# Optimization experiments

Measured on AMD Instinct MI355X. Metric: run time of the kernel, lower is better.

Reference implementation:

```python
import jax, jax.numpy as jnp
import numpy as np

NA, NT, A_DIM, E_DIM, L_LABELS, STEPS = 1024, 1024, 128, 128, 128, 2


def setup_inputs() -> dict:
    key = jax.random.key(0)
    k1, k2, k3, k4, k5 = jax.random.split(key, 5)
    return {
        "inputs": jax.random.randint(k1, (NA, NT), 0, L_LABELS, dtype=jnp.int32),
        "first_a": jax.random.normal(k2, (NA, A_DIM), dtype=jnp.float32),
        "first_t": jax.random.normal(k3, (NT, E_DIM), dtype=jnp.float32),
        "Awij": jax.random.normal(k4, (L_LABELS, A_DIM, E_DIM), dtype=jnp.float32),
        "Awij2": jax.random.normal(k5, (L_LABELS, E_DIM, A_DIM), dtype=jnp.float32),
    }


def _mp_step(update_a, update_t, inputs, Awij, Awij2):
    L = Awij.shape[0]
    # Phase A: a[j] += sum_t update_t[t] @ Awij2[inputs[j, t]]
    # Pre-contract task states with every label's weight matrix, then use
    # per-label 0/1 adjacency masks as dense GEMMs (compute-bound form of the
    # per-edge gather-multiply-accumulate in the original while loops).
    t_proj = jnp.einsum('te,lea->tla', update_t, Awij2)  # [Nt, L, A]

    def body_a(acc, l):
        mask = (inputs == l).astype(update_a.dtype)      # [Na, Nt]
        return acc + mask @ t_proj[:, l, :], None

    msg_a, _ = jax.lax.scan(body_a, jnp.zeros_like(update_a), jnp.arange(L))
    new_a = update_a + msg_a

    # Phase T: t[k] += sum_j new_a[j] @ Awij[inputs[j, k]] (uses updated a,
    # matching the loop order in the original body)
    a_proj = jnp.einsum('ja,lae->jle', new_a, Awij)      # [Na, L, E]

    def body_t(acc, l):
        mask = (inputs == l).astype(update_t.dtype)      # [Na, Nt]
        return acc + mask.T @ a_proj[:, l, :], None

    msg_t, _ = jax.lax.scan(body_t, jnp.zeros_like(update_t), jnp.arange(L))
    return new_a, update_t + msg_t


def reference(inputs, first_a, first_t, Awij, Awij2):
    a, t = first_a, first_t
    for _ in range(STEPS):
        a, t = _mp_step(a, t, inputs, Awij, Awij2)
    na, a_dim = a.shape
    nt, e_dim = t.shape
    top = jnp.concatenate([a, jnp.zeros((na, e_dim), a.dtype)], axis=1)
    bot = jnp.concatenate([t, jnp.zeros((nt, a_dim), t.dtype)], axis=1)
    return jnp.concatenate([top, bot], axis=0)  # [Na+Nt, A+E]
```

## Files before the change

kernel.cpp:

```cpp
#include <hip/hip_runtime.h>
#include <hip/hip_bf16.h>
#include <stdint.h>


typedef short bf16x8 __attribute__((ext_vector_type(8)));
typedef float f32x4  __attribute__((ext_vector_type(4)));

#define GLD16(g, l) __builtin_amdgcn_global_load_lds( \
    (const __attribute__((address_space(1))) void*)(uintptr_t)(g), \
    (__attribute__((address_space(3))) void*)(uintptr_t)(l), 16, 0, 0)

#define BF_LO(v) __uint_as_float((v) << 16)
#define BF_HI(v) __uint_as_float((v) & 0xffff0000u)

static __device__ __forceinline__ uint32_t pk2(float lo, float hi) {
    __hip_bfloat16 h0 = __float2bfloat16(lo), h1 = __float2bfloat16(hi);
    return ((uint32_t)(*(uint16_t*)&h1) << 16) | (uint32_t)(*(uint16_t*)&h0);
}

__global__ __launch_bounds__(256) void transpose_int_kernel(const int* __restrict__ in,
                                                            int* __restrict__ out) {
    __shared__ int tile[32][33];
    int b = blockIdx.x;
    int tr = b >> 5, tc = b & 31;
    int r0 = tr * 32, c0 = tc * 32;
    int tx = threadIdx.x & 31, ty = threadIdx.x >> 5;
#pragma unroll
    for (int p = 0; p < 4; ++p)
        tile[ty + p * 8][tx] = in[(size_t)(r0 + ty + p * 8) * 1024 + c0 + tx];
    __syncthreads();
#pragma unroll
    for (int p = 0; p < 4; ++p) {
        int cc = ty + p * 8;
        out[(size_t)(c0 + cc) * 1024 + r0 + tx] = tile[tx][cc];
    }
}

__global__ __launch_bounds__(256) void transpose_w_kernel(const float* __restrict__ W2,
                                                          const float* __restrict__ W1,
                                                          uint16_t* __restrict__ O2T,
                                                          uint16_t* __restrict__ O1T) {
    __shared__ float tile[32][33];
    int b = blockIdx.x;
    const float* W = W2;
    uint16_t* O = O2T;
    if (b >= 2048) { b -= 2048; W = W1; O = O1T; }
    int l = b >> 4, sub = b & 15;
    int x0 = (sub >> 2) * 32, y0 = (sub & 3) * 32;
    int tx = threadIdx.x & 31, ty = threadIdx.x >> 5;
#pragma unroll
    for (int p = 0; p < 4; ++p)
        tile[ty + p * 8][tx] = W[(size_t)l * 16384 + (size_t)(x0 + ty + p * 8) * 128 + y0 + tx];
    __syncthreads();
#pragma unroll
    for (int p = 0; p < 4; ++p) {
        int yy = ty + p * 8;
        __hip_bfloat16 h = __float2bfloat16(tile[tx][yy]);
        O[(size_t)(l * 128 + y0 + yy) * 128 + x0 + tx] = *(uint16_t*)&h;
    }
}

__global__ __launch_bounds__(256) void init_out_kernel(const float* __restrict__ fa,
                                                       const float* __restrict__ ft,
                                                       float* __restrict__ out,
                                                       uint16_t* __restrict__ srcAb,
                                                       uint16_t* __restrict__ srcTb) {
    int i = blockIdx.x * 256 + threadIdx.x;
    int r = i >> 8, c = i & 255;
    float v = 0.f;
    if (c < 128) {
        v = (r < 1024) ? fa[(size_t)r * 128 + c] : ft[(size_t)(r - 1024) * 128 + c];
        __hip_bfloat16 h = __float2bfloat16(v);
        if (r < 1024) srcAb[(size_t)r * 128 + c] = *(uint16_t*)&h;
        else          srcTb[(size_t)(r - 1024) * 128 + c] = *(uint16_t*)&h;
    }
    out[i] = v;
}

__global__ __launch_bounds__(512, 2) void proj_kernel(const uint16_t* __restrict__ src,
                                                      const uint16_t* __restrict__ WT,
                                                      uint16_t* __restrict__ proj) {
    __shared__ uint16_t At[128 * 128];
    __shared__ uint16_t Bt[128 * 128];

    const int tid = threadIdx.x;
    const int lane = tid & 63, wv = tid >> 6;
    const int bid = blockIdx.x;
    const int virt = (bid & 7) * 128 + (bid >> 3);
    const int mt = virt & 7;
    const int nt = virt >> 3;
    const int wr = wv >> 2, wc = wv & 3;

    const int rr = lane >> 4;
    const int sx16 = lane & 15;
#pragma unroll
    for (int g = 0; g < 4; ++g) {
        int row = wv * 16 + g * 4 + rr;
        int sx = sx16 ^ (row & 15);
        GLD16((const char*)src + ((size_t)(mt * 128 + row) * 128 + sx * 8) * 2,
              (char*)At + (wv * 16 + g * 4) * 256);
        GLD16((const char*)WT + ((size_t)(nt * 128 + row) * 128 + sx * 8) * 2,
              (char*)Bt + (wv * 16 + g * 4) * 256);
    }
    __syncthreads();

    f32x4 acc[4][2] = {};
    const int q = lane >> 4, rl = lane & 15;
#pragma unroll
    for (int kk = 0; kk < 4; ++kk) {
        bf16x8 af[4], bfr[2];
#pragma unroll
        for (int m = 0; m < 4; ++m) {
            int row = wr * 64 + m * 16 + rl;
            int sw = (kk * 4 + q) ^ (row & 15);
            af[m] = *(const bf16x8*)((const char*)At + row * 256 + sw * 16);
        }
#pragma unroll
        for (int n = 0; n < 2; ++n) {
            int row = wc * 32 + n * 16 + rl;
            int sw = (kk * 4 + q) ^ (row & 15);
            bfr[n] = *(const bf16x8*)((const char*)Bt + row * 256 + sw * 16);
        }
#pragma unroll
        for (int m = 0; m < 4; ++m)
#pragma unroll
            for (int n = 0; n < 2; ++n)
                acc[m][n] = __builtin_amdgcn_mfma_f32_16x16x32_bf16(bfr[n], af[m], acc[m][n], 0, 0, 0);
    }

#pragma unroll
    for (int m = 0; m < 4; ++m)
#pragma unroll
        for (int n = 0; n < 2; ++n) {
            int mrow = mt * 128 + wr * 64 + m * 16 + rl;
            int ncol = nt * 128 + wc * 32 + n * 16 + q * 4;
            uint2 pk;
            pk.x = pk2(acc[m][n][0], acc[m][n][1]);
            pk.y = pk2(acc[m][n][2], acc[m][n][3]);
            *(uint2*)(proj + (size_t)mrow * 16384 + ncol) = pk;
        }
}

__global__ __launch_bounds__(256, 8) void gather_partial_kernel(
    const int* __restrict__ labels,
    const uint32_t* __restrict__ proj,
    float* __restrict__ partial)
{
    __shared__ uint16_t lab16[128];
    __shared__ float red[4][128];
    const int bid = blockIdx.x;
    const int j = bid >> 3, ts = bid & 7;
    const int tid = threadIdx.x;
    const int lane = tid & 63, wv = tid >> 6;

    if (tid < 128) lab16[tid] = (uint16_t)labels[(size_t)j * 1024 + ts * 128 + tid];
    __syncthreads();

    float a0 = 0.f, a1 = 0.f, b0 = 0.f, b1 = 0.f;
    const uint32_t lane_u = (uint32_t)lane;
    const int t0 = ts * 128 + wv * 32;
#pragma unroll 1
    for (int i = 0; i < 32; i += 8) {
        ushort4 L0 = *(const ushort4*)&lab16[wv * 32 + i];
        ushort4 L1 = *(const ushort4*)&lab16[wv * 32 + i + 4];
        const uint32_t* base = proj + (size_t)(t0 + i) * 8192 + lane_u;
        uint32_t v0 = base[(uint32_t)L0.x * 64];
        uint32_t v1 = base[8192u + (uint32_t)L0.y * 64];
        uint32_t v2 = base[16384u + (uint32_t)L0.z * 64];
        uint32_t v3 = base[24576u + (uint32_t)L0.w * 64];
        uint32_t v4 = base[32768u + (uint32_t)L1.x * 64];
        uint32_t v5 = base[40960u + (uint32_t)L1.y * 64];
        uint32_t v6 = base[49152u + (uint32_t)L1.z * 64];
        uint32_t v7 = base[57344u + (uint32_t)L1.w * 64];
        a0 += BF_LO(v0) + BF_LO(v1) + BF_LO(v2) + BF_LO(v3);
        a1 += BF_HI(v0) + BF_HI(v1) + BF_HI(v2) + BF_HI(v3);
        b0 += BF_LO(v4) + BF_LO(v5) + BF_LO(v6) + BF_LO(v7);
        b1 += BF_HI(v4) + BF_HI(v5) + BF_HI(v6) + BF_HI(v7);
    }
    float2 pr;
    pr.x = a0 + b0;
    pr.y = a1 + b1;
    *(float2*)&red[wv][lane * 2] = pr;
    __syncthreads();

    if (tid < 128) {
        float s = (red[0][tid] + red[1][tid]) + (red[2][tid] + red[3][tid]);
        partial[((size_t)j * 8 + ts) * 128 + tid] = s;
    }
}

__global__ __launch_bounds__(256) void reduce_state_kernel(const float* __restrict__ partial,
                                                           float* __restrict__ state,
                                                           uint16_t* __restrict__ mirror) {
    int i = blockIdx.x * 256 + threadIdx.x;
    int j = i >> 7, c = i & 127;
    const float* p = partial + (size_t)j * 1024 + c;
    float s = ((p[0] + p[128]) + (p[256] + p[384])) + ((p[512] + p[640]) + (p[768] + p[896]));
    float v = state[(size_t)j * 256 + c] + s;
    state[(size_t)j * 256 + c] = v;
    __hip_bfloat16 h = __float2bfloat16(v);
    mirror[(size_t)j * 128 + c] = *(uint16_t*)&h;
}

extern "C" void kernel_launch(void* const* d_in, const int* in_sizes, int n_in,
                              void* d_out, int out_size, void* d_ws, size_t ws_size,
                              hipStream_t stream) {
    const int*   inputs  = (const int*)d_in[0];
    const float* first_a = (const float*)d_in[1];
    const float* first_t = (const float*)d_in[2];
    const float* Awij    = (const float*)d_in[3];
    const float* Awij2   = (const float*)d_in[4];
    float* out = (float*)d_out;

    char* w = (char*)d_ws;
    int*      inputsT = (int*)(w);
    uint16_t* W2T     = (uint16_t*)(w + (4u << 20));
    uint16_t* W1T     = (uint16_t*)(w + (8u << 20));
    uint16_t* srcAb   = (uint16_t*)(w + (12u << 20));
    uint16_t* srcTb   = (uint16_t*)(w + (12u << 20) + (1u << 19));
    float*    partial = (float*)(w + (13u << 20));
    uint16_t* proj16  = (uint16_t*)(w + (20u << 20));
    if (ws_size < (52u << 20)) return;

    float* stateA = out;
    float* stateT = out + 1024 * 256;

    transpose_int_kernel<<<1024, 256, 0, stream>>>(inputs, inputsT);
    transpose_w_kernel<<<4096, 256, 0, stream>>>(Awij2, Awij, W2T, W1T);
    init_out_kernel<<<2048, 256, 0, stream>>>(first_a, first_t, out, srcAb, srcTb);

    for (int s = 0; s < 2; ++s) {
        proj_kernel<<<1024, 512, 0, stream>>>(srcTb, W2T, proj16);
        gather_partial_kernel<<<8192, 256, 0, stream>>>(inputs, (const uint32_t*)proj16, partial);
        reduce_state_kernel<<<512, 256, 0, stream>>>(partial, stateA, srcAb);
        proj_kernel<<<1024, 512, 0, stream>>>(srcAb, W1T, proj16);
        gather_partial_kernel<<<8192, 256, 0, stream>>>(inputsT, (const uint32_t*)proj16, partial);
        reduce_state_kernel<<<512, 256, 0, stream>>>(partial, stateT, srcTb);
    }
}
```

Before: 170.1 us.

## Merge prep kernels, drop proj block swizzle, widen gather loads to 16

Folds the three setup kernels (label transpose, weight transpose and cast, output init) into one launch that branches on block index, which removes two kernel launches and their gaps. Drops the block-index remapping in the projection GEMM so blocks take M tiles in plain order. The gather kernel now issues 16 independent loads per iteration instead of 8, uses readfirstlane to keep the label offsets scalar, and keeps four accumulator pairs. This gives more memory-level parallelism in the gather at the cost of more registers, and changes the L2 locality pattern of the projection kernel.

```diff
diff --git a/kernel.cpp b/kernel.cpp
--- a/kernel.cpp
+++ b/kernel.cpp
@@ -18,63 +18,62 @@
     return ((uint32_t)(*(uint16_t*)&h1) << 16) | (uint32_t)(*(uint16_t*)&h0);
 }
 
-__global__ __launch_bounds__(256) void transpose_int_kernel(const int* __restrict__ in,
-                                                            int* __restrict__ out) {
-    __shared__ int tile[32][33];
-    int b = blockIdx.x;
-    int tr = b >> 5, tc = b & 31;
-    int r0 = tr * 32, c0 = tc * 32;
-    int tx = threadIdx.x & 31, ty = threadIdx.x >> 5;
-#pragma unroll
-    for (int p = 0; p < 4; ++p)
-        tile[ty + p * 8][tx] = in[(size_t)(r0 + ty + p * 8) * 1024 + c0 + tx];
-    __syncthreads();
-#pragma unroll
-    for (int p = 0; p < 4; ++p) {
-        int cc = ty + p * 8;
-        out[(size_t)(c0 + cc) * 1024 + r0 + tx] = tile[tx][cc];
-    }
-}
-
-__global__ __launch_bounds__(256) void transpose_w_kernel(const float* __restrict__ W2,
-                                                          const float* __restrict__ W1,
-                                                          uint16_t* __restrict__ O2T,
-                                                          uint16_t* __restrict__ O1T) {
+__global__ __launch_bounds__(256) void prep_kernel(const int* __restrict__ in,
+                                                   int* __restrict__ inT,
+                                                   const float* __restrict__ W2,
+                                                   const float* __restrict__ W1,
+                                                   uint16_t* __restrict__ O2T,
+                                                   uint16_t* __restrict__ O1T,
+                                                   const float* __restrict__ fa,
+                                                   const float* __restrict__ ft,
+                                                   float* __restrict__ out,
+                                                   uint16_t* __restrict__ srcAb,
+                                                   uint16_t* __restrict__ srcTb) {
     __shared__ float tile[32][33];
     int b = blockIdx.x;
-    const float* W = W2;
-    uint16_t* O = O2T;
-    if (b >= 2048) { b -= 2048; W = W1; O = O1T; }
-    int l = b >> 4, sub = b & 15;
-    int x0 = (sub >> 2) * 32, y0 = (sub & 3) * 32;
     int tx = threadIdx.x & 31, ty = threadIdx.x >> 5;
-#pragma unroll
-    for (int p = 0; p < 4; ++p)
-        tile[ty + p * 8][tx] = W[(size_t)l * 16384 + (size_t)(x0 + ty + p * 8) * 128 + y0 + tx];
-    __syncthreads();
-#pragma unroll
-    for (int p = 0; p < 4; ++p) {
-        int yy = ty + p * 8;
-        __hip_bfloat16 h = __float2bfloat16(tile[tx][yy]);
-        O[(size_t)(l * 128 + y0 + yy) * 128 + x0 + tx] = *(uint16_t*)&h;
-    }
-}
-
-__global__ __launch_bounds__(256) void init_out_kernel(const float* __restrict__ fa,
-                                                       const float* __restrict__ ft,
-                                                       float* __restrict__ out,
-                                                       uint16_t* __restrict__ srcAb,
-                                                       uint16_t* __restrict__ srcTb) {
-    int i = blockIdx.x * 256 + threadIdx.x;
-    int r = i >> 8, c = i & 255;
-    float v = 0.f;
-    if (c < 128) {
-        v = (r < 1024) ? fa[(size_t)r * 128 + c] : ft[(size_t)(r - 1024) * 128 + c];
-        __hip_bfloat16 h = __float2bfloat16(v);
-        if (r < 1024) srcAb[(size_t)r * 128 + c] = *(uint16_t*)&h;
-        else          srcTb[(size_t)(r - 1024) * 128 + c] = *(uint16_t*)&h;
-    }
-    out[i] = v;
+
+    if (b < 1024) {
+        int tr = b >> 5, tc = b & 31;
+        int r0 = tr * 32, c0 = tc * 32;
+#pragma unroll
+        for (int p = 0; p < 4; ++p)
+            tile[ty + p * 8][tx] = __int_as_float(in[(size_t)(r0 + ty + p * 8) * 1024 + c0 + tx]);
+        __syncthreads();
+#pragma unroll
+        for (int p = 0; p < 4; ++p) {
+            int cc = ty + p * 8;
+            inT[(size_t)(c0 + cc) * 1024 + r0 + tx] = __float_as_int(tile[tx][cc]);
+        }
+    } else if (b < 5120) {
+        int bb = b - 1024;
+        const float* W = W2;
+        uint16_t* O = O2T;
+        if (bb >= 2048) { bb -= 2048; W = W1; O = O1T; }
+        int l = bb >> 4, sub = bb & 15;
+        int x0 = (sub >> 2) * 32, y0 = (sub & 3) * 32;
+#pragma unroll
+        for (int p = 0; p < 4; ++p)
+            tile[ty + p * 8][tx] = W[(size_t)l * 16384 + (size_t)(x0 + ty + p * 8) * 128 + y0 + tx];
+        __syncthreads();
+#pragma unroll
+        for (int p = 0; p < 4; ++p) {
+            int yy = ty + p * 8;
+            __hip_bfloat16 h = __float2bfloat16(tile[tx][yy]);
+            O[(size_t)(l * 128 + y0 + yy) * 128 + x0 + tx] = *(uint16_t*)&h;
+        }
+    } else {
+        int i = (b - 5120) * 256 + threadIdx.x;
+        int r = i >> 8, c = i & 255;
+        float v = 0.f;
+        if (c < 128) {
+            v = (r < 1024) ? fa[(size_t)r * 128 + c] : ft[(size_t)(r - 1024) * 128 + c];
+            __hip_bfloat16 h = __float2bfloat16(v);
+            if (r < 1024) srcAb[(size_t)r * 128 + c] = *(uint16_t*)&h;
+            else          srcTb[(size_t)(r - 1024) * 128 + c] = *(uint16_t*)&h;
+        }
+        out[i] = v;
+    }
 }
 
 __global__ __launch_bounds__(512, 2) void proj_kernel(const uint16_t* __restrict__ src,
@@ -86,9 +85,8 @@
     const int tid = threadIdx.x;
     const int lane = tid & 63, wv = tid >> 6;
     const int bid = blockIdx.x;
-    const int virt = (bid & 7) * 128 + (bid >> 3);
-    const int mt = virt & 7;
-    const int nt = virt >> 3;
+    const int mt = bid & 7;
+    const int nt = bid >> 3;
     const int wr = wv >> 2, wc = wv & 3;
 
     const int rr = lane >> 4;
@@ -156,30 +154,39 @@
     if (tid < 128) lab16[tid] = (uint16_t)labels[(size_t)j * 1024 + ts * 128 + tid];
     __syncthreads();
 
+    const uint32_t lane_u = (uint32_t)lane;
+    const uint32_t* tb = proj + (size_t)(ts * 128 + wv * 32) * 8192 + lane_u;
     float a0 = 0.f, a1 = 0.f, b0 = 0.f, b1 = 0.f;
-    const uint32_t lane_u = (uint32_t)lane;
-    const int t0 = ts * 128 + wv * 32;
+    float c0 = 0.f, c1 = 0.f, d0 = 0.f, d1 = 0.f;
+
 #pragma unroll 1
-    for (int i = 0; i < 32; i += 8) {
-        ushort4 L0 = *(const ushort4*)&lab16[wv * 32 + i];
-        ushort4 L1 = *(const ushort4*)&lab16[wv * 32 + i + 4];
-        const uint32_t* base = proj + (size_t)(t0 + i) * 8192 + lane_u;
-        uint32_t v0 = base[(uint32_t)L0.x * 64];
-        uint32_t v1 = base[8192u + (uint32_t)L0.y * 64];
-        uint32_t v2 = base[16384u + (uint32_t)L0.z * 64];
-        uint32_t v3 = base[24576u + (uint32_t)L0.w * 64];
-        uint32_t v4 = base[32768u + (uint32_t)L1.x * 64];
-        uint32_t v5 = base[40960u + (uint32_t)L1.y * 64];
-        uint32_t v6 = base[49152u + (uint32_t)L1.z * 64];
-        uint32_t v7 = base[57344u + (uint32_t)L1.w * 64];
-        a0 += BF_LO(v0) + BF_LO(v1) + BF_LO(v2) + BF_LO(v3);
-        a1 += BF_HI(v0) + BF_HI(v1) + BF_HI(v2) + BF_HI(v3);
-        b0 += BF_LO(v4) + BF_LO(v5) + BF_LO(v6) + BF_LO(v7);
-        b1 += BF_HI(v4) + BF_HI(v5) + BF_HI(v6) + BF_HI(v7);
+    for (int i = 0; i < 32; i += 16) {
+        int L[16];
+#pragma unroll
+        for (int g = 0; g < 4; ++g) {
+            ushort4 q = *(const ushort4*)&lab16[wv * 32 + i + g * 4];
+            L[g * 4 + 0] = __builtin_amdgcn_readfirstlane((int)q.x);
+            L[g * 4 + 1] = __builtin_amdgcn_readfirstlane((int)q.y);
+            L[g * 4 + 2] = __builtin_amdgcn_readfirstlane((int)q.z);
+            L[g * 4 + 3] = __builtin_amdgcn_readfirstlane((int)q.w);
+        }
+        uint32_t v[16];
+#pragma unroll
+        for (int e = 0; e < 16; ++e)
+            v[e] = tb[(uint32_t)(i + e) * 8192u + (uint32_t)L[e] * 64u];
+
+        a0 += BF_LO(v[0]) + BF_LO(v[1]) + BF_LO(v[2]) + BF_LO(v[3]);
+        a1 += BF_HI(v[0]) + BF_HI(v[1]) + BF_HI(v[2]) + BF_HI(v[3]);
+        b0 += BF_LO(v[4]) + BF_LO(v[5]) + BF_LO(v[6]) + BF_LO(v[7]);
+        b1 += BF_HI(v[4]) + BF_HI(v[5]) + BF_HI(v[6]) + BF_HI(v[7]);
+        c0 += BF_LO(v[8]) + BF_LO(v[9]) + BF_LO(v[10]) + BF_LO(v[11]);
+        c1 += BF_HI(v[8]) + BF_HI(v[9]) + BF_HI(v[10]) + BF_HI(v[11]);
+        d0 += BF_LO(v[12]) + BF_LO(v[13]) + BF_LO(v[14]) + BF_LO(v[15]);
+        d1 += BF_HI(v[12]) + BF_HI(v[13]) + BF_HI(v[14]) + BF_HI(v[15]);
     }
     float2 pr;
-    pr.x = a0 + b0;
-    pr.y = a1 + b1;
+    pr.x = (a0 + b0) + (c0 + d0);
+    pr.y = (a1 + b1) + (c1 + d1);
     *(float2*)&red[wv][lane * 2] = pr;
     __syncthreads();
 
@@ -225,9 +232,8 @@
     float* stateA = out;
     float* stateT = out + 1024 * 256;
 
-    transpose_int_kernel<<<1024, 256, 0, stream>>>(inputs, inputsT);
-    transpose_w_kernel<<<4096, 256, 0, stream>>>(Awij2, Awij, W2T, W1T);
-    init_out_kernel<<<2048, 256, 0, stream>>>(first_a, first_t, out, srcAb, srcTb);
+    prep_kernel<<<7168, 256, 0, stream>>>(inputs, inputsT, Awij2, Awij, W2T, W1T,
+                                          first_a, first_t, out, srcAb, srcTb);
 
     for (int s = 0; s < 2; ++s) {
         proj_kernel<<<1024, 512, 0, stream>>>(srcTb, W2T, proj16);
```

New measurement: 168.5 us. Within noise of the previous version (-1.0%).
